# Kernel optimization log

Measured on AMD Instinct MI355X. Metric: run time of the kernel, lower is better.

Reference implementation:

```python
import jax, jax.numpy as jnp
import numpy as np

B, R, L, K = 64, 196, 512, 768
NEG = jnp.float32(-2**31 + 1)


def setup_inputs() -> dict:
    key = jax.random.key(0)
    ks = jax.random.split(key, 8)
    image_emb = jax.random.normal(ks[0], (B, R, L), dtype=jnp.float32)
    seq_emb = jax.random.normal(ks[1], (B, L, K), dtype=jnp.float32)
    mask = jax.random.randint(ks[2], (B, L), 0, 2, dtype=jnp.int32)
    # Linear(l,1) and Linear(k,1) params, Xavier-ish scale
    image_W = jax.random.normal(ks[3], (L, 1), dtype=jnp.float32) / np.sqrt(L)
    image_b = jnp.zeros((1,), dtype=jnp.float32)
    seq_W = jax.random.normal(ks[4], (K, 1), dtype=jnp.float32) / np.sqrt(K)
    seq_b = jnp.zeros((1,), dtype=jnp.float32)
    # V_weight [L, L], xavier_uniform
    lim = np.sqrt(6.0 / (L + L)).astype(np.float32)
    V_weight = jax.random.uniform(ks[5], (L, L), dtype=jnp.float32, minval=-lim, maxval=lim)
    return {"image_emb": image_emb, "seq_emb": seq_emb, "mask": mask,
            "image_W": image_W, "image_b": image_b,
            "seq_W": seq_W, "seq_b": seq_b, "V_weight": V_weight}


def reference(image_emb, seq_emb, mask, image_W, image_b, seq_W, seq_b, V_weight):
    # p: [B,R,1], q: [B,L,1]
    p = jnp.tanh(image_emb @ image_W + image_b)
    q = jnp.tanh(seq_emb @ seq_W + seq_b)
    qt = jnp.swapaxes(q, 1, 2)              # [B,1,L]
    emb = p @ qt + qt                       # [B,R,L] (rank-1 outer + broadcast add)
    score = emb @ V_weight                  # [B,R,L]
    # dropout_rate=0.0 -> identity
    score = jnp.where(mask[:, None, :] == 0, NEG, score)
    score = jax.nn.softmax(score, axis=-1)  # [B,R,L]
    out = score @ seq_emb                   # [B,R,K]
    out = out / jnp.sqrt(jnp.float32(seq_emb.shape[-1]))
    return out
```

## Files before the change

kernel.cpp:

```cpp
#include <hip/hip_runtime.h>
#include <cstdint>
#include <cstddef>


typedef __attribute__((ext_vector_type(8))) short short8;
typedef __attribute__((ext_vector_type(4))) float f32x4;

__device__ __forceinline__ unsigned short f32_to_bf16(float x) {
    unsigned int u = __float_as_uint(x);
    unsigned int r = (u + 0x7FFFu + ((u >> 16) & 1u)) >> 16;
    return (unsigned short)r;
}
__device__ __forceinline__ float bf16_to_f32(unsigned short h) {
    return __uint_as_float(((unsigned int)h) << 16);
}

#if defined(__has_builtin)
#if __has_builtin(__builtin_amdgcn_cvt_pk_bf16_f32)
#define HAVE_PK_BF16 1
#endif
#endif

__device__ __forceinline__ unsigned int pk_bf16(float a, float b) {
#ifdef HAVE_PK_BF16
    typedef __attribute__((ext_vector_type(2))) __bf16 bf16x2;
    bf16x2 v = __builtin_amdgcn_cvt_pk_bf16_f32(a, b);
    return __builtin_bit_cast(unsigned int, v);
#else
    return (unsigned int)f32_to_bf16(a) | ((unsigned int)f32_to_bf16(b) << 16);
#endif
}

__global__ __launch_bounds__(256) void kprep(const float* __restrict__ seq,
                                             const float* __restrict__ seqW,
                                             const float* __restrict__ img,
                                             const float* __restrict__ imgW,
                                             const float* __restrict__ imgBias,
                                             unsigned short* __restrict__ seqT,
                                             float* __restrict__ qacc,
                                             float* __restrict__ pv) {
    __shared__ __align__(16) unsigned int sT[128 * 32];
    __shared__ __align__(16) float sWc[128];

    if (blockIdx.x >= 3072) {
        int wv = threadIdx.x >> 6, lane = threadIdx.x & 63;
        int row = (blockIdx.x - 3072) * 4 + wv;
        const float4* x4 = (const float4*)(img + (size_t)row * 512);
        const float4* w4 = (const float4*)imgW;
        float s = 0.f;
#pragma unroll
        for (int i = 0; i < 2; ++i) {
            float4 a = x4[i * 64 + lane];
            float4 c = w4[i * 64 + lane];
            s += a.x * c.x + a.y * c.y + a.z * c.z + a.w * c.w;
        }
#pragma unroll
        for (int o = 32; o; o >>= 1) s += __shfl_xor(s, o, 64);
        if (lane == 0) pv[row] = tanhf(s + imgBias[0]);
        return;
    }

    int id = blockIdx.x;
    int b = id / 48, rem = id - b * 48;
    int jt = rem / 6, ck = rem - jt * 6;
    int j0 = jt * 64;
    int t = threadIdx.x;
    if (t < 128) sWc[t] = seqW[ck * 128 + t];

    int quad = t >> 4, kseg = t & 15;
    int qk = quad ^ kseg;
    const float* base = seq + (size_t)b * 512 * 768 + (size_t)(j0 + quad * 4) * 768 + ck * 128;
    int jg = t & 7, krow = t >> 3;
    float qp[4] = {0.f, 0.f, 0.f, 0.f};
    __syncthreads();

#pragma unroll
    for (int rp = 0; rp < 2; ++rp) {
        int kq = rp * 64 + kseg * 4;
        float4 r0 = *(const float4*)(base + 0 * 768 + kq);
        float4 r1 = *(const float4*)(base + 1 * 768 + kq);
        float4 r2 = *(const float4*)(base + 2 * 768 + kq);
        float4 r3 = *(const float4*)(base + 3 * 768 + kq);
        float4 w  = *(const float4*)(sWc + kq);
        qp[0] += r0.x * w.x + r0.y * w.y + r0.z * w.z + r0.w * w.w;
        qp[1] += r1.x * w.x + r1.y * w.y + r1.z * w.z + r1.w * w.w;
        qp[2] += r2.x * w.x + r2.y * w.y + r2.z * w.z + r2.w * w.w;
        qp[3] += r3.x * w.x + r3.y * w.y + r3.z * w.z + r3.w * w.w;
        float a0[4] = {r0.x, r0.y, r0.z, r0.w};
        float a1[4] = {r1.x, r1.y, r1.z, r1.w};
        float a2[4] = {r2.x, r2.y, r2.z, r2.w};
        float a3[4] = {r3.x, r3.y, r3.z, r3.w};
#pragma unroll
        for (int i = 0; i < 4; ++i) {
            int k = kq + i;
            int col = (qk ^ (i << 2)) & 15;
            uint2 v;
            v.x = pk_bf16(a0[i], a1[i]);
            v.y = pk_bf16(a2[i], a3[i]);
            *(uint2*)(sT + k * 32 + col * 2) = v;
        }
    }
    __syncthreads();
    unsigned short* dst = seqT + (size_t)b * 768 * 512 + (size_t)ck * 128 * 512 + j0;
#pragma unroll
    for (int wp = 0; wp < 4; ++wp) {
        int k = wp * 32 + krow;
        int s = ((k >> 2) & 15) ^ ((k & 3) << 2);
        int c0 = ((jg << 1) ^ s) & 15;
        int c1 = ((jg << 1) ^ 1 ^ s) & 15;
        uint2 va = *(const uint2*)(sT + k * 32 + c0 * 2);
        uint2 vb = *(const uint2*)(sT + k * 32 + c1 * 2);
        uint4 o;
        o.x = va.x; o.y = va.y; o.z = vb.x; o.w = vb.y;
        *(uint4*)(dst + (size_t)k * 512 + jg * 8) = o;
    }
#pragma unroll
    for (int rr = 0; rr < 4; ++rr) {
        float s = qp[rr];
        s += __shfl_xor(s, 8, 64);
        s += __shfl_xor(s, 4, 64);
        s += __shfl_xor(s, 2, 64);
        s += __shfl_xor(s, 1, 64);
        if (kseg == 0) atomicAdd(qacc + b * 512 + j0 + quad * 4 + rr, s);
    }
}

__global__ __launch_bounds__(256) void krows_p(const float* __restrict__ x,
                                               const float* __restrict__ w,
                                               const float* __restrict__ bias,
                                               float* __restrict__ outp) {
    int wv = threadIdx.x >> 6, lane = threadIdx.x & 63;
    int row = blockIdx.x * 4 + wv;
    const float4* x4 = (const float4*)(x + (size_t)row * 512);
    const float4* w4 = (const float4*)w;
    float s = 0.f;
#pragma unroll
    for (int i = 0; i < 2; ++i) {
        float4 a = x4[i * 64 + lane];
        float4 c = w4[i * 64 + lane];
        s += a.x * c.x + a.y * c.y + a.z * c.z + a.w * c.w;
    }
#pragma unroll
    for (int o = 32; o; o >>= 1) s += __shfl_xor(s, o, 64);
    if (lane == 0) outp[row] = tanhf(s + bias[0]);
}

__global__ __launch_bounds__(256) void krows_q(const float* __restrict__ x,
                                               const float* __restrict__ w,
                                               float* __restrict__ outp) {
    int wv = threadIdx.x >> 6, lane = threadIdx.x & 63;
    int row = blockIdx.x * 4 + wv;
    const float4* x4 = (const float4*)(x + (size_t)row * 768);
    const float4* w4 = (const float4*)w;
    float s = 0.f;
#pragma unroll
    for (int i = 0; i < 3; ++i) {
        float4 a = x4[i * 64 + lane];
        float4 c = w4[i * 64 + lane];
        s += a.x * c.x + a.y * c.y + a.z * c.z + a.w * c.w;
    }
#pragma unroll
    for (int o = 32; o; o >>= 1) s += __shfl_xor(s, o, 64);
    if (lane == 0) outp[row] = s;
}

__global__ __launch_bounds__(256) void kw(const float* __restrict__ qacc,
                                          const float* __restrict__ seqBias,
                                          const float* __restrict__ V,
                                          const int* __restrict__ mask,
                                          float* __restrict__ wm) {
    __shared__ __align__(16) float sq[512];
    __shared__ __align__(16) float sacc[8][32][4];
    int b = blockIdx.x >> 2, jc = blockIdx.x & 3;
    int t = threadIdx.x;
    float qb = seqBias[0];
    sq[t] = tanhf(qacc[b * 512 + t] + qb);
    sq[t + 256] = tanhf(qacc[b * 512 + t + 256] + qb);
    __syncthreads();
    int jt = t & 31, lg = t >> 5;
    const float4* V4 = (const float4*)V;
    int col4 = jc * 32 + jt;
    float ax = 0.f, ay = 0.f, az = 0.f, aw = 0.f;
    int lbase = lg * 64;
#pragma unroll 8
    for (int li = 0; li < 64; ++li) {
        int l = lbase + li;
        float qq = sq[l];
        float4 v = V4[(size_t)l * 128 + col4];
        ax += qq * v.x; ay += qq * v.y; az += qq * v.z; aw += qq * v.w;
    }
    sacc[lg][jt][0] = ax; sacc[lg][jt][1] = ay;
    sacc[lg][jt][2] = az; sacc[lg][jt][3] = aw;
    __syncthreads();
    if (t < 32) {
        float sx = 0.f, sy = 0.f, sz = 0.f, sw = 0.f;
#pragma unroll
        for (int g = 0; g < 8; ++g) {
            sx += sacc[g][t][0]; sy += sacc[g][t][1];
            sz += sacc[g][t][2]; sw += sacc[g][t][3];
        }
        const int* mrow = mask + b * 512 + jc * 128 + t * 4;
        float4 o;
        o.x = mrow[0] ? sx : -1e30f;
        o.y = mrow[1] ? sy : -1e30f;
        o.z = mrow[2] ? sz : -1e30f;
        o.w = mrow[3] ? sw : -1e30f;
        ((float4*)(wm + b * 512 + jc * 128))[t] = o;
    }
}

__global__ __launch_bounds__(256, 2) void kattn2(const unsigned short* __restrict__ seqT,
                                                 const float* __restrict__ p,
                                                 const float* __restrict__ wm,
                                                 float* __restrict__ out) {
    __shared__ __align__(16) unsigned short sB[2][128 * 64];
    __shared__ __align__(16) float swm[512];
    __shared__ float sinvz[64];
    __shared__ float sred[16];

    int raw = blockIdx.x;
    int g  = ((raw >> 5) << 3) + (raw & 7);
    int rt = (raw >> 3) & 3;
    int b  = g / 6, nt = g - b * 6;
    int t  = threadIdx.x;
    int wv = t >> 6, lane = t & 63;
    int mm = lane & 15, q = lane >> 4;
    int nb = nt * 128;

    float v0 = wm[b * 512 + t];
    float v1 = wm[b * 512 + t + 256];
    swm[t] = v0; swm[t + 256] = v1;
    float lmax = fmaxf(v0, v1);
    float fa = (v0 > -1e29f) ? v0 : 1e30f;
    float fb = (v1 > -1e29f) ? v1 : 1e30f;
    float lmin = fminf(fa, fb);
#pragma unroll
    for (int o = 32; o; o >>= 1) {
        lmax = fmaxf(lmax, __shfl_xor(lmax, o, 64));
        lmin = fminf(lmin, __shfl_xor(lmin, o, 64));
    }
    if (lane == 0) { sred[wv] = lmax; sred[8 + wv] = lmin; }
    __syncthreads();
    float wmax = fmaxf(fmaxf(sred[0], sred[1]), fmaxf(sred[2], sred[3]));
    float wmin = fminf(fminf(sred[8], sred[9]), fminf(sred[10], sred[11]));

    int rl = wv * 16 + mm;
    int r  = rt * 64 + rl;
    bool valid = r < 196;
    int pidx = b * 196 + (valid ? r : 195);
    float c = 1.0f + p[pidx];
    float M = (c >= 0.f) ? c * wmax : c * wmin;

    short8 afrag[16];
    float zsum = 0.f;
    const f32x4* swm4 = (const f32x4*)swm;
#pragma unroll
    for (int tk = 0; tk < 16; ++tk) {
        int jb = tk * 32 + q * 8;
        f32x4 w0 = swm4[jb >> 2];
        f32x4 w1 = swm4[(jb >> 2) + 1];
        short8 af;
#pragma unroll
        for (int jj = 0; jj < 8; ++jj) {
            float ww = (jj < 4) ? w0[jj] : w1[jj - 4];
            float e = valid ? __expf(c * ww - M) : 0.f;
            unsigned short h = f32_to_bf16(e);
            zsum += bf16_to_f32(h);
            af[jj] = (short)h;
        }
        afrag[tk] = af;
    }
    zsum += __shfl_xor(zsum, 16, 64);
    zsum += __shfl_xor(zsum, 32, 64);
    if (q == 0) sinvz[rl] = 1.0f / zsum;

    f32x4 acc[8];
#pragma unroll
    for (int s = 0; s < 8; ++s) acc[s] = (f32x4){0.f, 0.f, 0.f, 0.f};

    const unsigned short* seqTb = seqT + (size_t)b * 768 * 512 + (size_t)nb * 512;
    int nrow = t >> 3, jg = t & 7;
    auto stage = [&](int ch, int buf) {
        unsigned short* sb = sB[buf];
#pragma unroll
        for (int pp = 0; pp < 4; ++pp) {
            int n = pp * 32 + nrow;
            short8 v = *(const short8*)(seqTb + (size_t)n * 512 + ch * 64 + jg * 8);
            int sw = (n ^ (n >> 3)) & 7;
            *(short8*)(sb + n * 64 + ((jg ^ sw) << 3)) = v;
        }
    };

    __syncthreads();
    stage(0, 0);
    __syncthreads();
#pragma unroll
    for (int ch = 0; ch < 8; ++ch) {
        if (ch < 7) stage(ch + 1, (ch + 1) & 1);
        const unsigned short* cb = sB[ch & 1];
#pragma unroll
        for (int kk = 0; kk < 2; ++kk) {
            short8 bfr[8];
#pragma unroll
            for (int s = 0; s < 8; ++s) {
                int n = s * 16 + mm;
                int sw = (n ^ (n >> 3)) & 7;
                bfr[s] = *(const short8*)(cb + n * 64 + ((((kk << 2) + q) ^ sw) << 3));
            }
#pragma unroll
            for (int s = 0; s < 8; ++s)
                acc[s] = __builtin_amdgcn_mfma_f32_16x16x32_bf16(
                    afrag[(ch << 1) + kk], bfr[s], acc[s], 0, 0, 0);
        }
        __syncthreads();
    }

    const float invsqrtk = 0.036084391824351615f;
#pragma unroll
    for (int reg = 0; reg < 4; ++reg) {
        int row = q * 4 + reg;
        int rr = rt * 64 + wv * 16 + row;
        if (rr < 196) {
            float scale = sinvz[wv * 16 + row] * invsqrtk;
            float* op = out + (size_t)(b * 196 + rr) * 768 + nb + mm;
#pragma unroll
            for (int s = 0; s < 8; ++s)
                op[s * 16] = acc[s][reg] * scale;
        }
    }
}

__global__ __launch_bounds__(256, 2) void kattn(const float* __restrict__ seq,
                                                const float* __restrict__ p,
                                                const float* __restrict__ wm,
                                                float* __restrict__ out) {
    __shared__ __align__(16) unsigned int sseq[2][128 * 32];
    __shared__ __align__(16) float swm[512];
    __shared__ float sinvz[64];
    __shared__ float sred[16];

    int id = blockIdx.x;
    int rt = id & 3;
    int nt = (id >> 2) % 6;
    int b  = id / 24;
    int t  = threadIdx.x;
    int wv = t >> 6, lane = t & 63;
    int mm = lane & 15, q = lane >> 4;
    int nb = nt * 128;

    float v0 = wm[b * 512 + t];
    float v1 = wm[b * 512 + t + 256];
    swm[t] = v0; swm[t + 256] = v1;
    float lmax = fmaxf(v0, v1);
    float fa = (v0 > -1e29f) ? v0 : 1e30f;
    float fb = (v1 > -1e29f) ? v1 : 1e30f;
    float lmin = fminf(fa, fb);
#pragma unroll
    for (int o = 32; o; o >>= 1) {
        lmax = fmaxf(lmax, __shfl_xor(lmax, o, 64));
        lmin = fminf(lmin, __shfl_xor(lmin, o, 64));
    }
    if (lane == 0) { sred[wv] = lmax; sred[8 + wv] = lmin; }
    __syncthreads();
    float wmax = fmaxf(fmaxf(sred[0], sred[1]), fmaxf(sred[2], sred[3]));
    float wmin = fminf(fminf(sred[8], sred[9]), fminf(sred[10], sred[11]));

    int rl = wv * 16 + mm;
    int r  = rt * 64 + rl;
    bool valid = r < 196;
    int pidx = b * 196 + (valid ? r : 195);
    float c = 1.0f + p[pidx];
    float M = (c >= 0.f) ? c * wmax : c * wmin;

    short8 afrag[16];
    float zsum = 0.f;
    const f32x4* swm4 = (const f32x4*)swm;
#pragma unroll
    for (int tk = 0; tk < 16; ++tk) {
        int jb = tk * 32 + q * 8;
        f32x4 w0 = swm4[jb >> 2];
        f32x4 w1 = swm4[(jb >> 2) + 1];
        short8 af;
#pragma unroll
        for (int jj = 0; jj < 8; ++jj) {
            float ww = (jj < 4) ? w0[jj] : w1[jj - 4];
            float e = valid ? __expf(c * ww - M) : 0.f;
            unsigned short h = f32_to_bf16(e);
            zsum += bf16_to_f32(h);
            af[jj] = (short)h;
        }
        afrag[tk] = af;
    }
    zsum += __shfl_xor(zsum, 16, 64);
    zsum += __shfl_xor(zsum, 32, 64);
    if (q == 0) sinvz[rl] = 1.0f / zsum;

    f32x4 acc[8];
#pragma unroll
    for (int s = 0; s < 8; ++s) acc[s] = (f32x4){0.f, 0.f, 0.f, 0.f};

    const float* seqb = seq + (size_t)b * 512 * 768 + nb;
    int tl = t & 31, jp = t >> 5;
    int n0 = tl * 4;
    auto stage = [&](int ch, int buf) {
        unsigned int* sb = sseq[buf];
#pragma unroll
        for (int pass = 0; pass < 4; ++pass) {
            int jl = pass * 16 + jp * 2;
            int jglob = ch * 64 + jl;
            float4 a0 = *(const float4*)(seqb + (size_t)jglob * 768 + n0);
            float4 a1 = *(const float4*)(seqb + (size_t)(jglob + 1) * 768 + n0);
            float a0v[4] = {a0.x, a0.y, a0.z, a0.w};
            float a1v[4] = {a1.x, a1.y, a1.z, a1.w};
            int g = jl >> 3;
            int wo = (jl & 7) >> 1;
#pragma unroll
            for (int i = 0; i < 4; ++i) {
                int n = n0 + i;
                int sw = (n ^ (n >> 3)) & 7;
                unsigned int pk = (unsigned int)f32_to_bf16(a0v[i]) |
                                  ((unsigned int)f32_to_bf16(a1v[i]) << 16);
                sb[n * 32 + ((g ^ sw) << 2) + wo] = pk;
            }
        }
    };

    __syncthreads();
    stage(0, 0);
    __syncthreads();
#pragma unroll
    for (int ch = 0; ch < 8; ++ch) {
        if (ch < 7) stage(ch + 1, (ch + 1) & 1);
        const unsigned int* cb = sseq[ch & 1];
#pragma unroll
        for (int kk = 0; kk < 2; ++kk) {
            short8 bfr[8];
#pragma unroll
            for (int s = 0; s < 8; ++s) {
                int n = s * 16 + mm;
                int g = kk * 4 + q;
                int sw = (n ^ (n >> 3)) & 7;
                bfr[s] = *(const short8*)(cb + n * 32 + ((g ^ sw) << 2));
            }
#pragma unroll
            for (int s = 0; s < 8; ++s)
                acc[s] = __builtin_amdgcn_mfma_f32_16x16x32_bf16(
                    afrag[ch * 2 + kk], bfr[s], acc[s], 0, 0, 0);
        }
        __syncthreads();
    }

    const float invsqrtk = 0.036084391824351615f;
#pragma unroll
    for (int reg = 0; reg < 4; ++reg) {
        int row = q * 4 + reg;
        int rr = rt * 64 + wv * 16 + row;
        if (rr < 196) {
            float scale = sinvz[wv * 16 + row] * invsqrtk;
            float* op = out + (size_t)(b * 196 + rr) * 768 + nb + mm;
#pragma unroll
            for (int s = 0; s < 8; ++s)
                op[s * 16] = acc[s][reg] * scale;
        }
    }
}

extern "C" void kernel_launch(void* const* d_in, const int* in_sizes, int n_in,
                              void* d_out, int out_size, void* d_ws, size_t ws_size,
                              hipStream_t stream) {
    const float* image_emb = (const float*)d_in[0];
    const float* seq_emb   = (const float*)d_in[1];
    const int*   mask      = (const int*)d_in[2];
    const float* image_W   = (const float*)d_in[3];
    const float* image_b   = (const float*)d_in[4];
    const float* seq_W     = (const float*)d_in[5];
    const float* seq_b     = (const float*)d_in[6];
    const float* V         = (const float*)d_in[7];
    float* out = (float*)d_out;

    float* p_ws  = (float*)d_ws;
    float* q_ws  = (float*)((char*)d_ws + (64 << 10));
    float* wm_ws = (float*)((char*)d_ws + (192 << 10));
    unsigned short* seqT = (unsigned short*)((char*)d_ws + (384 << 10));

    size_t need = (size_t)(384 << 10) + (size_t)64 * 768 * 512 * 2;
    if (ws_size >= need) {
        hipMemsetAsync(q_ws, 0, 512 * 64 * sizeof(float), stream);
        kprep<<<dim3(6208), dim3(256), 0, stream>>>(seq_emb, seq_W,
                                                    image_emb, image_W, image_b,
                                                    seqT, q_ws, p_ws);
        kw<<<dim3(256), dim3(256), 0, stream>>>(q_ws, seq_b, V, mask, wm_ws);
        kattn2<<<dim3(1536), dim3(256), 0, stream>>>(seqT, p_ws, wm_ws, out);
    } else {
        krows_p<<<dim3(3136), dim3(256), 0, stream>>>(image_emb, image_W, image_b, p_ws);
        krows_q<<<dim3(8192), dim3(256), 0, stream>>>(seq_emb, seq_W, q_ws);
        kw<<<dim3(256), dim3(256), 0, stream>>>(q_ws, seq_b, V, mask, wm_ws);
        kattn<<<dim3(1536), dim3(256), 0, stream>>>(seq_emb, p_ws, wm_ws, out);
    }
}
```

Measured before the change: 235.9 us.

## Replace q atomics with per-chunk partial buffers and skip idle waves in kattn2

kprep now writes per-K-chunk partial dot products into separate slices instead of calling atomicAdd, and kw sums the slices itself. This removes the memset launch and atomic contention. kattn2 also skips the exp/softmax fragment build and the MFMA work for waves whose 16-row slab lies entirely past row 196, while still joining the barriers. The cost is a larger workspace and a few extra loads in kw.

```diff
diff --git a/kernel.cpp b/kernel.cpp
--- a/kernel.cpp
+++ b/kernel.cpp
@@ -37,7 +37,7 @@
                                              const float* __restrict__ imgW,
                                              const float* __restrict__ imgBias,
                                              unsigned short* __restrict__ seqT,
-                                             float* __restrict__ qacc,
+                                             float* __restrict__ qpart,
                                              float* __restrict__ pv) {
     __shared__ __align__(16) unsigned int sT[128 * 32];
     __shared__ __align__(16) float sWc[128];
@@ -121,7 +121,8 @@
         s += __shfl_xor(s, 4, 64);
         s += __shfl_xor(s, 2, 64);
         s += __shfl_xor(s, 1, 64);
-        if (kseg == 0) atomicAdd(qacc + b * 512 + j0 + quad * 4 + rr, s);
+        if (kseg == 0)
+            qpart[(size_t)ck * 32768 + b * 512 + j0 + quad * 4 + rr] = s;
     }
 }
 
@@ -164,18 +165,24 @@
     if (lane == 0) outp[row] = s;
 }
 
-__global__ __launch_bounds__(256) void kw(const float* __restrict__ qacc,
+__global__ __launch_bounds__(256) void kw(const float* __restrict__ qpart,
                                           const float* __restrict__ seqBias,
                                           const float* __restrict__ V,
                                           const int* __restrict__ mask,
-                                          float* __restrict__ wm) {
+                                          float* __restrict__ wm,
+                                          int nparts) {
     __shared__ __align__(16) float sq[512];
     __shared__ __align__(16) float sacc[8][32][4];
     int b = blockIdx.x >> 2, jc = blockIdx.x & 3;
     int t = threadIdx.x;
     float qb = seqBias[0];
-    sq[t] = tanhf(qacc[b * 512 + t] + qb);
-    sq[t + 256] = tanhf(qacc[b * 512 + t + 256] + qb);
+    float a0 = 0.f, a1 = 0.f;
+    for (int pp = 0; pp < nparts; ++pp) {
+        a0 += qpart[(size_t)pp * 32768 + b * 512 + t];
+        a1 += qpart[(size_t)pp * 32768 + b * 512 + t + 256];
+    }
+    sq[t] = tanhf(a0 + qb);
+    sq[t + 256] = tanhf(a1 + qb);
     __syncthreads();
     int jt = t & 31, lg = t >> 5;
     const float4* V4 = (const float4*)V;
@@ -241,38 +248,43 @@
     }
     if (lane == 0) { sred[wv] = lmax; sred[8 + wv] = lmin; }
     __syncthreads();
-    float wmax = fmaxf(fmaxf(sred[0], sred[1]), fmaxf(sred[2], sred[3]));
-    float wmin = fminf(fminf(sred[8], sred[9]), fminf(sred[10], sred[11]));
+
+    bool wactive = (rt * 64 + wv * 16) < 196;
 
     int rl = wv * 16 + mm;
     int r  = rt * 64 + rl;
     bool valid = r < 196;
-    int pidx = b * 196 + (valid ? r : 195);
-    float c = 1.0f + p[pidx];
-    float M = (c >= 0.f) ? c * wmax : c * wmin;
 
     short8 afrag[16];
-    float zsum = 0.f;
-    const f32x4* swm4 = (const f32x4*)swm;
-#pragma unroll
-    for (int tk = 0; tk < 16; ++tk) {
-        int jb = tk * 32 + q * 8;
-        f32x4 w0 = swm4[jb >> 2];
-        f32x4 w1 = swm4[(jb >> 2) + 1];
-        short8 af;
-#pragma unroll
-        for (int jj = 0; jj < 8; ++jj) {
-            float ww = (jj < 4) ? w0[jj] : w1[jj - 4];
-            float e = valid ? __expf(c * ww - M) : 0.f;
-            unsigned short h = f32_to_bf16(e);
-            zsum += bf16_to_f32(h);
-            af[jj] = (short)h;
-        }
-        afrag[tk] = af;
-    }
-    zsum += __shfl_xor(zsum, 16, 64);
-    zsum += __shfl_xor(zsum, 32, 64);
-    if (q == 0) sinvz[rl] = 1.0f / zsum;
+    if (wactive) {
+        float wmax = fmaxf(fmaxf(sred[0], sred[1]), fmaxf(sred[2], sred[3]));
+        float wmin = fminf(fminf(sred[8], sred[9]), fminf(sred[10], sred[11]));
+        int pidx = b * 196 + (valid ? r : 195);
+        float c = 1.0f + p[pidx];
+        float M = (c >= 0.f) ? c * wmax : c * wmin;
+
+        float zsum = 0.f;
+        const f32x4* swm4 = (const f32x4*)swm;
+#pragma unroll
+        for (int tk = 0; tk < 16; ++tk) {
+            int jb = tk * 32 + q * 8;
+            f32x4 w0 = swm4[jb >> 2];
+            f32x4 w1 = swm4[(jb >> 2) + 1];
+            short8 af;
+#pragma unroll
+            for (int jj = 0; jj < 8; ++jj) {
+                float ww = (jj < 4) ? w0[jj] : w1[jj - 4];
+                float e = valid ? __expf(c * ww - M) : 0.f;
+                unsigned short h = f32_to_bf16(e);
+                zsum += bf16_to_f32(h);
+                af[jj] = (short)h;
+            }
+            afrag[tk] = af;
+        }
+        zsum += __shfl_xor(zsum, 16, 64);
+        zsum += __shfl_xor(zsum, 32, 64);
+        if (q == 0) sinvz[rl] = 1.0f / zsum;
+    }
 
     f32x4 acc[8];
 #pragma unroll
@@ -297,35 +309,39 @@
 #pragma unroll
     for (int ch = 0; ch < 8; ++ch) {
         if (ch < 7) stage(ch + 1, (ch + 1) & 1);
-        const unsigned short* cb = sB[ch & 1];
-#pragma unroll
-        for (int kk = 0; kk < 2; ++kk) {
-            short8 bfr[8];
-#pragma unroll
-            for (int s = 0; s < 8; ++s) {
-                int n = s * 16 + mm;
-                int sw = (n ^ (n >> 3)) & 7;
-                bfr[s] = *(const short8*)(cb + n * 64 + ((((kk << 2) + q) ^ sw) << 3));
+        if (wactive) {
+            const unsigned short* cb = sB[ch & 1];
+#pragma unroll
+            for (int kk = 0; kk < 2; ++kk) {
+                short8 bfr[8];
+#pragma unroll
+                for (int s = 0; s < 8; ++s) {
+                    int n = s * 16 + mm;
+                    int sw = (n ^ (n >> 3)) & 7;
+                    bfr[s] = *(const short8*)(cb + n * 64 + ((((kk << 2) + q) ^ sw) << 3));
+                }
+#pragma unroll
+                for (int s = 0; s < 8; ++s)
+                    acc[s] = __builtin_amdgcn_mfma_f32_16x16x32_bf16(
+                        afrag[(ch << 1) + kk], bfr[s], acc[s], 0, 0, 0);
             }
-#pragma unroll
-            for (int s = 0; s < 8; ++s)
-                acc[s] = __builtin_amdgcn_mfma_f32_16x16x32_bf16(
-                    afrag[(ch << 1) + kk], bfr[s], acc[s], 0, 0, 0);
         }
         __syncthreads();
     }
 
-    const float invsqrtk = 0.036084391824351615f;
-#pragma unroll
-    for (int reg = 0; reg < 4; ++reg) {
-        int row = q * 4 + reg;
-        int rr = rt * 64 + wv * 16 + row;
-        if (rr < 196) {
-            float scale = sinvz[wv * 16 + row] * invsqrtk;
-            float* op = out + (size_t)(b * 196 + rr) * 768 + nb + mm;
-#pragma unroll
-            for (int s = 0; s < 8; ++s)
-                op[s * 16] = acc[s][reg] * scale;
+    if (wactive) {
+        const float invsqrtk = 0.036084391824351615f;
+#pragma unroll
+        for (int reg = 0; reg < 4; ++reg) {
+            int row = q * 4 + reg;
+            int rr = rt * 64 + wv * 16 + row;
+            if (rr < 196) {
+                float scale = sinvz[wv * 16 + row] * invsqrtk;
+                float* op = out + (size_t)(b * 196 + rr) * 768 + nb + mm;
+#pragma unroll
+                for (int s = 0; s < 8; ++s)
+                    op[s * 16] = acc[s][reg] * scale;
+            }
         }
     }
 }
@@ -479,22 +495,21 @@
     float* out = (float*)d_out;
 
     float* p_ws  = (float*)d_ws;
-    float* q_ws  = (float*)((char*)d_ws + (64 << 10));
-    float* wm_ws = (float*)((char*)d_ws + (192 << 10));
-    unsigned short* seqT = (unsigned short*)((char*)d_ws + (384 << 10));
-
-    size_t need = (size_t)(384 << 10) + (size_t)64 * 768 * 512 * 2;
+    float* qpart = (float*)((char*)d_ws + (128 << 10));
+    float* wm_ws = (float*)((char*)d_ws + (896 << 10));
+    unsigned short* seqT = (unsigned short*)((char*)d_ws + (1024 << 10));
+
+    size_t need = (size_t)(1024 << 10) + (size_t)64 * 768 * 512 * 2;
     if (ws_size >= need) {
-        hipMemsetAsync(q_ws, 0, 512 * 64 * sizeof(float), stream);
         kprep<<<dim3(6208), dim3(256), 0, stream>>>(seq_emb, seq_W,
                                                     image_emb, image_W, image_b,
-                                                    seqT, q_ws, p_ws);
-        kw<<<dim3(256), dim3(256), 0, stream>>>(q_ws, seq_b, V, mask, wm_ws);
+                                                    seqT, qpart, p_ws);
+        kw<<<dim3(256), dim3(256), 0, stream>>>(qpart, seq_b, V, mask, wm_ws, 6);
         kattn2<<<dim3(1536), dim3(256), 0, stream>>>(seqT, p_ws, wm_ws, out);
     } else {
         krows_p<<<dim3(3136), dim3(256), 0, stream>>>(image_emb, image_W, image_b, p_ws);
-        krows_q<<<dim3(8192), dim3(256), 0, stream>>>(seq_emb, seq_W, q_ws);
-        kw<<<dim3(256), dim3(256), 0, stream>>>(q_ws, seq_b, V, mask, wm_ws);
+        krows_q<<<dim3(8192), dim3(256), 0, stream>>>(seq_emb, seq_W, qpart);
+        kw<<<dim3(256), dim3(256), 0, stream>>>(qpart, seq_b, V, mask, wm_ws, 1);
         kattn<<<dim3(1536), dim3(256), 0, stream>>>(seq_emb, p_ws, wm_ws, out);
     }
 }
```

New measurement: 235.4 us. Within noise of the previous version (-0.2%).
